# Kernel tuning notes

Measured on AMD Instinct MI355X. Metric: run time of the kernel, lower is better.

## Reference

```python
import jax, jax.numpy as jnp
import numpy as np

V = 100000   # num_regular_embeddings (full vocab)
K = 20000    # num custom (Poincare) embeddings
P = 300      # custom embedding dim
E = 256      # regular / output embedding dim
B = 1024
L = 256


def logmap0(v):
    # project from Poincare ball (c=1) to tangent space at origin
    norm = jnp.linalg.norm(v, axis=-1, keepdims=True)
    safe = jnp.where(norm > 0, norm, 0.5)            # avoid 0/0 and arctanh(0)/0
    scale = jnp.where(norm > 0, jnp.arctanh(safe) / safe, 1.0)
    return scale * v


def mobius_add(x, y):
    x2 = jnp.sum(x * x, axis=-1, keepdims=True)
    y2 = jnp.sum(y * y, axis=-1, keepdims=True)
    xy = jnp.sum(x * y, axis=-1, keepdims=True)
    num = (1 + 2 * xy + y2) * x + (1 - x2) * y
    denom = jnp.maximum(1 + 2 * xy + x2 * y2, 1e-15)
    return num / denom


def setup_inputs() -> dict:
    key = jax.random.key(0)
    k_x, k_perm, k_cw, k_rw, k_lw = jax.random.split(key, 5)

    x = jax.random.randint(k_x, (B, L), 0, V, dtype=jnp.int32)

    # K distinct custom vocab indices, excluding 0 (padding)
    custom_indices = jax.random.permutation(k_perm, jnp.arange(1, V, dtype=jnp.int32))[:K]

    # vocab -> custom table index (1..K), 0 for non-custom
    vocab_to_custom = jnp.zeros((V,), dtype=jnp.int32).at[custom_indices].set(
        jnp.arange(1, K + 1, dtype=jnp.int32))
    # vocab -> regular table index (0..V-K-1) for non-custom slots
    regular_vocab = jnp.where(vocab_to_custom == 0)[0]  # concrete, size V-K
    vocab_to_regular = jnp.zeros((V,), dtype=jnp.int32).at[regular_vocab].set(
        jnp.arange(V - K, dtype=jnp.int32))

    # fixed (pretrained, frozen) custom weights inside unit ball; row 0 = padding
    custom_fixed_w = (jax.random.normal(k_cw, (K + 1, P), dtype=jnp.float32) * 0.02).at[0].set(0.0)
    # trainable custom table initialized to zeros (as in the module)
    custom_train_w = jnp.zeros((K + 1, P), dtype=jnp.float32)
    # regular embedding table, row 0 = padding
    regular_w = (jax.random.normal(k_rw, (V - K, E), dtype=jnp.float32) * 0.02).at[0].set(0.0)
    # linear transform P -> E
    lin_w = jax.random.normal(k_lw, (E, P), dtype=jnp.float32) * 0.05
    lin_b = jnp.zeros((E,), dtype=jnp.float32)

    return {"x": x, "custom_indices": custom_indices,
            "vocab_to_custom": vocab_to_custom, "vocab_to_regular": vocab_to_regular,
            "custom_fixed_w": custom_fixed_w, "custom_train_w": custom_train_w,
            "regular_w": regular_w, "lin_w": lin_w, "lin_b": lin_b}


def reference(x, custom_indices, vocab_to_custom, vocab_to_regular,
              custom_fixed_w, custom_train_w, regular_w, lin_w, lin_b):
    mask = jnp.isin(x, custom_indices)                     # [B, L]
    custom_feat = jnp.where(mask, x, 0)
    regular_feat = jnp.where(mask, 0, x)

    cm = vocab_to_custom[custom_feat]                      # [B, L]
    fixed = logmap0(custom_fixed_w[cm])                    # [B, L, P]
    train = custom_train_w[cm]                             # [B, L, P]
    custom_emb = mobius_add(fixed, train)                  # [B, L, P]

    regular_emb = regular_w[vocab_to_regular[regular_feat]]  # [B, L, E]

    custom_emb = jnp.einsum("blp,ep->ble", custom_emb, lin_w) + lin_b
    return custom_emb + regular_emb
```

## Files before the change

kernel.cpp:

```cpp
#include <hip/hip_runtime.h>
#include <stdint.h>
#include <math.h>

#define NTOK (1024 * 256)
#define P_DIM 300
#define P_PAD 320
#define P_LDS 328
#define E_DIM 256

typedef __attribute__((ext_vector_type(8))) short bf16x8_t;
typedef __attribute__((ext_vector_type(4))) float f32x4_t;

__device__ __forceinline__ unsigned short f2b(float f) {
    union { float f; unsigned int i; } v; v.f = f;
    unsigned int x = v.i;
    return (unsigned short)((x + 0x7FFFu + ((x >> 16) & 1u)) >> 16);
}

__global__ __launch_bounds__(256) void k1_classify(
        const int* __restrict__ x, const int* __restrict__ v2c,
        const int* __restrict__ v2r,
        int* __restrict__ info, int* __restrict__ list, int* __restrict__ counter) {
    __shared__ int wb[4];
    int tid = threadIdx.x;
    int wid = tid >> 6;
    int lane = tid & 63;
    int base = blockIdx.x * 1024;

    int cmv[4], tv[4];
    unsigned long long bl[4];
    int wcnt = 0;
    #pragma unroll
    for (int it = 0; it < 4; it++) {
        int t = base + it * 256 + tid;
        int xv = x[t];
        int cm = v2c[xv];
        cmv[it] = cm; tv[it] = t;
        info[t] = (cm > 0) ? -cm : v2r[xv];
        bl[it] = __ballot(cm > 0);
        wcnt += __popcll(bl[it]);
    }
    if (lane == 0) wb[wid] = wcnt;
    __syncthreads();
    if (tid == 0) {
        int tot = wb[0] + wb[1] + wb[2] + wb[3];
        int b0 = atomicAdd(counter, tot);
        int p = b0;
        #pragma unroll
        for (int w = 0; w < 4; w++) { int c = wb[w]; wb[w] = p; p += c; }
    }
    __syncthreads();
    int off = wb[wid];
    unsigned long long lmask = (1ull << lane) - 1ull;
    #pragma unroll
    for (int it = 0; it < 4; it++) {
        if (cmv[it] > 0) {
            int pos = off + __popcll(bl[it] & lmask);
            list[pos] = tv[it];
        }
        off += __popcll(bl[it]);
    }
}

__global__ __launch_bounds__(256) void k2_base(
        const int* __restrict__ info,
        const float* __restrict__ regular_w,
        const float* __restrict__ lin_b,
        const float* __restrict__ lin_w,
        unsigned short* __restrict__ lin_w_pad,
        float* __restrict__ out) {
    int tid = threadIdx.x;
    if (blockIdx.x < (E_DIM * P_PAD) / 256) {
        int idx = blockIdx.x * 256 + tid;
        int e = idx / P_PAD;
        int k = idx - e * P_PAD;
        lin_w_pad[idx] = (k < P_DIM) ? f2b(lin_w[e * P_DIM + k]) : (unsigned short)0;
    }
    int lane = tid & 63;
    int wq = tid >> 6;
    float4 lb = *(const float4*)(lin_b + lane * 4);
    int base = blockIdx.x * 32;
    #pragma unroll
    for (int it = 0; it < 8; it++) {
        int t = base + wq * 8 + it;
        int inf = info[t];
        if (inf >= 0) {
            float4 rf = *(const float4*)(regular_w + (size_t)inf * E_DIM + lane * 4);
            float4 o;
            o.x = rf.x + lb.x; o.y = rf.y + lb.y;
            o.z = rf.z + lb.z; o.w = rf.w + lb.w;
            *(float4*)(out + (size_t)t * E_DIM + lane * 4) = o;
        }
    }
}

__global__ __launch_bounds__(256) void k3_gemm(
        const int* __restrict__ list, const int* __restrict__ counter,
        const int* __restrict__ info, const int* __restrict__ v2r,
        const float* __restrict__ fixed_w,
        const float* __restrict__ train_w,
        const unsigned short* __restrict__ lin_w_pad,
        const float* __restrict__ regular_w,
        const float* __restrict__ lin_b,
        float* __restrict__ out) {
    __shared__ __align__(16) unsigned short semb[32][P_LDS];
    int count = counter[0];
    int i0 = blockIdx.x * 32;
    if (i0 >= count) return;
    int tid = threadIdx.x;
    int wid = tid >> 6;
    int lane = tid & 63;

    for (int it = 0; it < 8; it++) {
        int i = i0 + wid * 8 + it;
        int iS = (i < count) ? i : (count - 1);
        int t = list[iS];
        int cm = -info[t];
        const float* fw = fixed_w + (size_t)cm * P_DIM;
        const float* tw = train_w + (size_t)cm * P_DIM;
        float w[5], tr[5];
        float sw2 = 0.f, st2 = 0.f, swt = 0.f;
        #pragma unroll
        for (int s = 0; s < 5; s++) {
            int j = lane + 64 * s;
            float wv = 0.f, tv = 0.f;
            if (j < P_DIM) { wv = fw[j]; tv = tw[j]; }
            w[s] = wv; tr[s] = tv;
            sw2 = fmaf(wv, wv, sw2); st2 = fmaf(tv, tv, st2); swt = fmaf(wv, tv, swt);
        }
        #pragma unroll
        for (int m = 32; m >= 1; m >>= 1) {
            sw2 += __shfl_xor(sw2, m, 64);
            st2 += __shfl_xor(st2, m, 64);
            swt += __shfl_xor(swt, m, 64);
        }
        float norm = sqrtf(sw2);
        norm = fminf(norm, 0.9999999f);
        float scale = (norm > 0.f) ? (atanhf(norm) / norm) : 1.0f;
        float x2 = scale * scale * sw2;
        float y2 = st2;
        float xy = scale * swt;
        float c1 = (1.f + 2.f * xy + y2) * scale;
        float c2 = (1.f - x2);
        float den = fmaxf(1.f + 2.f * xy + x2 * y2, 1e-15f);
        float inv = 1.f / den;
        int tl = wid * 8 + it;
        #pragma unroll
        for (int s = 0; s < 5; s++) {
            int j = lane + 64 * s;
            float v = (j < P_DIM) ? (c1 * w[s] + c2 * tr[s]) * inv : 0.f;
            semb[tl][j] = f2b(v);
        }
    }
    __syncthreads();

    int col = lane & 15;
    int kgrp = lane >> 4;
    int e0w = wid * 64;
    f32x4_t acc[2][4];
    #pragma unroll
    for (int a = 0; a < 2; a++)
        #pragma unroll
        for (int b = 0; b < 4; b++) acc[a][b] = (f32x4_t)(0.f);

    #pragma unroll
    for (int kk = 0; kk < 10; kk++) {
        int k0 = kk * 32 + kgrp * 8;
        bf16x8_t afr[2], bfr[4];
        #pragma unroll
        for (int mt = 0; mt < 2; mt++)
            afr[mt] = *(const bf16x8_t*)(&semb[mt * 16 + col][k0]);
        #pragma unroll
        for (int nt = 0; nt < 4; nt++) {
            int e = e0w + nt * 16 + col;
            bfr[nt] = *(const bf16x8_t*)(lin_w_pad + (size_t)e * P_PAD + k0);
        }
        #pragma unroll
        for (int mt = 0; mt < 2; mt++)
            #pragma unroll
            for (int nt = 0; nt < 4; nt++)
                acc[mt][nt] = __builtin_amdgcn_mfma_f32_16x16x32_bf16(
                    afr[mt], bfr[nt], acc[mt][nt], 0, 0, 0);
    }

    int rid0 = v2r[0];
    const float* rrow0 = regular_w + (size_t)rid0 * E_DIM;
    float lb[4];
    #pragma unroll
    for (int nt = 0; nt < 4; nt++) lb[nt] = lin_b[e0w + nt * 16 + col];
    int rbase = (lane >> 4) * 4;
    #pragma unroll
    for (int mt = 0; mt < 2; mt++) {
        #pragma unroll
        for (int r = 0; r < 4; r++) {
            int i = i0 + mt * 16 + rbase + r;
            if (i < count) {
                int t = list[i];
                float* orow = out + (size_t)t * E_DIM;
                #pragma unroll
                for (int nt = 0; nt < 4; nt++) {
                    int e = e0w + nt * 16 + col;
                    orow[e] = acc[mt][nt][r] + lb[nt] + rrow0[e];
                }
            }
        }
    }
}

extern "C" void kernel_launch(void* const* d_in, const int* in_sizes, int n_in,
                              void* d_out, int out_size, void* d_ws, size_t ws_size,
                              hipStream_t stream) {
    const int* x   = (const int*)d_in[0];
    const int* v2c = (const int*)d_in[2];
    const int* v2r = (const int*)d_in[3];
    const float* fixed_w   = (const float*)d_in[4];
    const float* train_w   = (const float*)d_in[5];
    const float* regular_w = (const float*)d_in[6];
    const float* lin_w     = (const float*)d_in[7];
    const float* lin_b     = (const float*)d_in[8];
    float* out = (float*)d_out;

    char* ws = (char*)d_ws;
    int* counter = (int*)ws;
    int* info    = (int*)(ws + 256);
    int* list    = (int*)(ws + 256 + 4 * (size_t)NTOK);
    unsigned short* lin_w_pad = (unsigned short*)(ws + 256 + 8 * (size_t)NTOK);

    hipMemsetAsync(counter, 0, 64, stream);
    k1_classify<<<NTOK / 1024, 256, 0, stream>>>(x, v2c, v2r, info, list, counter);
    k2_base<<<NTOK / 32, 256, 0, stream>>>(info, regular_w, lin_b, lin_w,
                                           lin_w_pad, out);
    k3_gemm<<<NTOK / 32, 256, 0, stream>>>(list, counter, info, v2r,
                                           fixed_w, train_w, lin_w_pad,
                                           regular_w, lin_b, out);
}
```

Before: 452.6 us.

## Fuse classify, regular gather and custom GEMM into one per-block kernel

New measurement: 542.7 us. +19.9%, slower.

```diff
diff --git a/kernel.cpp b/kernel.cpp
--- a/kernel.cpp
+++ b/kernel.cpp
@@ -3,6 +3,7 @@
 #include <math.h>
 
 #define NTOK (1024 * 256)
+#define TPB  128
 #define P_DIM 300
 #define P_PAD 320
 #define P_LDS 328
@@ -17,193 +18,167 @@
     return (unsigned short)((x + 0x7FFFu + ((x >> 16) & 1u)) >> 16);
 }
 
-__global__ __launch_bounds__(256) void k1_classify(
+__global__ __launch_bounds__(256) void k0_convert(
+        const float* __restrict__ lin_w, unsigned short* __restrict__ lin_w_pad) {
+    int idx = blockIdx.x * 256 + threadIdx.x;
+    int e = idx / P_PAD;
+    int k = idx - e * P_PAD;
+    lin_w_pad[idx] = (k < P_DIM) ? f2b(lin_w[(size_t)e * P_DIM + k]) : (unsigned short)0;
+}
+
+__global__ __launch_bounds__(256) void k_fused(
         const int* __restrict__ x, const int* __restrict__ v2c,
         const int* __restrict__ v2r,
-        int* __restrict__ info, int* __restrict__ list, int* __restrict__ counter) {
-    __shared__ int wb[4];
-    int tid = threadIdx.x;
-    int wid = tid >> 6;
-    int lane = tid & 63;
-    int base = blockIdx.x * 1024;
-
-    int cmv[4], tv[4];
-    unsigned long long bl[4];
-    int wcnt = 0;
-    #pragma unroll
-    for (int it = 0; it < 4; it++) {
-        int t = base + it * 256 + tid;
-        int xv = x[t];
-        int cm = v2c[xv];
-        cmv[it] = cm; tv[it] = t;
-        info[t] = (cm > 0) ? -cm : v2r[xv];
-        bl[it] = __ballot(cm > 0);
-        wcnt += __popcll(bl[it]);
-    }
-    if (lane == 0) wb[wid] = wcnt;
-    __syncthreads();
-    if (tid == 0) {
-        int tot = wb[0] + wb[1] + wb[2] + wb[3];
-        int b0 = atomicAdd(counter, tot);
-        int p = b0;
-        #pragma unroll
-        for (int w = 0; w < 4; w++) { int c = wb[w]; wb[w] = p; p += c; }
-    }
-    __syncthreads();
-    int off = wb[wid];
-    unsigned long long lmask = (1ull << lane) - 1ull;
-    #pragma unroll
-    for (int it = 0; it < 4; it++) {
-        if (cmv[it] > 0) {
-            int pos = off + __popcll(bl[it] & lmask);
-            list[pos] = tv[it];
-        }
-        off += __popcll(bl[it]);
-    }
-}
-
-__global__ __launch_bounds__(256) void k2_base(
-        const int* __restrict__ info,
-        const float* __restrict__ regular_w,
-        const float* __restrict__ lin_b,
-        const float* __restrict__ lin_w,
-        unsigned short* __restrict__ lin_w_pad,
-        float* __restrict__ out) {
-    int tid = threadIdx.x;
-    if (blockIdx.x < (E_DIM * P_PAD) / 256) {
-        int idx = blockIdx.x * 256 + tid;
-        int e = idx / P_PAD;
-        int k = idx - e * P_PAD;
-        lin_w_pad[idx] = (k < P_DIM) ? f2b(lin_w[e * P_DIM + k]) : (unsigned short)0;
-    }
-    int lane = tid & 63;
-    int wq = tid >> 6;
-    float4 lb = *(const float4*)(lin_b + lane * 4);
-    int base = blockIdx.x * 32;
-    #pragma unroll
-    for (int it = 0; it < 8; it++) {
-        int t = base + wq * 8 + it;
-        int inf = info[t];
-        if (inf >= 0) {
-            float4 rf = *(const float4*)(regular_w + (size_t)inf * E_DIM + lane * 4);
-            float4 o;
-            o.x = rf.x + lb.x; o.y = rf.y + lb.y;
-            o.z = rf.z + lb.z; o.w = rf.w + lb.w;
-            *(float4*)(out + (size_t)t * E_DIM + lane * 4) = o;
-        }
-    }
-}
-
-__global__ __launch_bounds__(256) void k3_gemm(
-        const int* __restrict__ list, const int* __restrict__ counter,
-        const int* __restrict__ info, const int* __restrict__ v2r,
         const float* __restrict__ fixed_w,
         const float* __restrict__ train_w,
+        const float* __restrict__ regular_w,
         const unsigned short* __restrict__ lin_w_pad,
-        const float* __restrict__ regular_w,
         const float* __restrict__ lin_b,
         float* __restrict__ out) {
     __shared__ __align__(16) unsigned short semb[32][P_LDS];
-    int count = counter[0];
-    int i0 = blockIdx.x * 32;
-    if (i0 >= count) return;
-    int tid = threadIdx.x;
-    int wid = tid >> 6;
+    __shared__ int stok[TPB];
+    __shared__ int scm[TPB];
+    __shared__ int rinfo[TPB];
+    __shared__ int s_n;
+
+    int tid  = threadIdx.x;
+    int wid  = tid >> 6;
     int lane = tid & 63;
-
-    for (int it = 0; it < 8; it++) {
-        int i = i0 + wid * 8 + it;
-        int iS = (i < count) ? i : (count - 1);
-        int t = list[iS];
-        int cm = -info[t];
-        const float* fw = fixed_w + (size_t)cm * P_DIM;
-        const float* tw = train_w + (size_t)cm * P_DIM;
-        float w[5], tr[5];
-        float sw2 = 0.f, st2 = 0.f, swt = 0.f;
-        #pragma unroll
-        for (int s = 0; s < 5; s++) {
-            int j = lane + 64 * s;
-            float wv = 0.f, tv = 0.f;
-            if (j < P_DIM) { wv = fw[j]; tv = tw[j]; }
-            w[s] = wv; tr[s] = tv;
-            sw2 = fmaf(wv, wv, sw2); st2 = fmaf(tv, tv, st2); swt = fmaf(wv, tv, swt);
-        }
-        #pragma unroll
-        for (int m = 32; m >= 1; m >>= 1) {
-            sw2 += __shfl_xor(sw2, m, 64);
-            st2 += __shfl_xor(st2, m, 64);
-            swt += __shfl_xor(swt, m, 64);
-        }
-        float norm = sqrtf(sw2);
-        norm = fminf(norm, 0.9999999f);
-        float scale = (norm > 0.f) ? (atanhf(norm) / norm) : 1.0f;
-        float x2 = scale * scale * sw2;
-        float y2 = st2;
-        float xy = scale * swt;
-        float c1 = (1.f + 2.f * xy + y2) * scale;
-        float c2 = (1.f - x2);
-        float den = fmaxf(1.f + 2.f * xy + x2 * y2, 1e-15f);
-        float inv = 1.f / den;
-        int tl = wid * 8 + it;
-        #pragma unroll
-        for (int s = 0; s < 5; s++) {
-            int j = lane + 64 * s;
-            float v = (j < P_DIM) ? (c1 * w[s] + c2 * tr[s]) * inv : 0.f;
-            semb[tl][j] = f2b(v);
-        }
-    }
+    int base = blockIdx.x * TPB;
+
+    if (tid == 0) s_n = 0;
     __syncthreads();
 
-    int col = lane & 15;
+    if (tid < TPB) {
+        int t  = base + tid;
+        int xv = x[t];
+        int cm = v2c[xv];
+        int ri = -1;
+        if (cm > 0) {
+            int p = atomicAdd(&s_n, 1);
+            stok[p] = t;
+            scm[p]  = cm;
+        } else {
+            ri = v2r[xv];
+        }
+        rinfo[tid] = ri;
+    }
+    __syncthreads();
+    int n = s_n;
+
+    f32x4_t lb4 = *(const f32x4_t*)(lin_b + lane * 4);
+    #pragma unroll 4
+    for (int it = 0; it < TPB / 4; it++) {
+        int li = wid * (TPB / 4) + it;
+        int ri = rinfo[li];
+        if (ri >= 0) {
+            f32x4_t rf = *(const f32x4_t*)(regular_w + (size_t)ri * E_DIM + lane * 4);
+            f32x4_t o = rf + lb4;
+            __builtin_nontemporal_store(
+                o, (f32x4_t*)(out + (size_t)(base + li) * E_DIM + lane * 4));
+        }
+    }
+
+    if (n == 0) return;
+
+    int col  = lane & 15;
     int kgrp = lane >> 4;
-    int e0w = wid * 64;
-    f32x4_t acc[2][4];
-    #pragma unroll
-    for (int a = 0; a < 2; a++)
-        #pragma unroll
-        for (int b = 0; b < 4; b++) acc[a][b] = (f32x4_t)(0.f);
-
-    #pragma unroll
-    for (int kk = 0; kk < 10; kk++) {
-        int k0 = kk * 32 + kgrp * 8;
-        bf16x8_t afr[2], bfr[4];
-        #pragma unroll
-        for (int mt = 0; mt < 2; mt++)
-            afr[mt] = *(const bf16x8_t*)(&semb[mt * 16 + col][k0]);
-        #pragma unroll
-        for (int nt = 0; nt < 4; nt++) {
-            int e = e0w + nt * 16 + col;
-            bfr[nt] = *(const bf16x8_t*)(lin_w_pad + (size_t)e * P_PAD + k0);
-        }
-        #pragma unroll
-        for (int mt = 0; mt < 2; mt++)
-            #pragma unroll
-            for (int nt = 0; nt < 4; nt++)
-                acc[mt][nt] = __builtin_amdgcn_mfma_f32_16x16x32_bf16(
-                    afr[mt], bfr[nt], acc[mt][nt], 0, 0, 0);
-    }
-
+    int e0w  = wid * 64;
+    int rbase = kgrp * 4;
+    float lbe[4], rr0[4];
     int rid0 = v2r[0];
     const float* rrow0 = regular_w + (size_t)rid0 * E_DIM;
-    float lb[4];
     #pragma unroll
-    for (int nt = 0; nt < 4; nt++) lb[nt] = lin_b[e0w + nt * 16 + col];
-    int rbase = (lane >> 4) * 4;
-    #pragma unroll
-    for (int mt = 0; mt < 2; mt++) {
+    for (int nt = 0; nt < 4; nt++) {
+        lbe[nt] = lin_b[e0w + nt * 16 + col];
+        rr0[nt] = rrow0[e0w + nt * 16 + col];
+    }
+
+    for (int c0 = 0; c0 < n; c0 += 32) {
+        int cn = n - c0; if (cn > 32) cn = 32;
+
+        for (int i = wid; i < cn; i += 4) {
+            int cm = scm[c0 + i];
+            const float* fw = fixed_w + (size_t)cm * P_DIM;
+            const float* tw = train_w + (size_t)cm * P_DIM;
+            float w[5], tr[5];
+            float sw2 = 0.f, st2 = 0.f, swt = 0.f;
+            #pragma unroll
+            for (int s = 0; s < 5; s++) {
+                int j = lane + 64 * s;
+                float wv = 0.f, tv = 0.f;
+                if (j < P_DIM) { wv = fw[j]; tv = tw[j]; }
+                w[s] = wv; tr[s] = tv;
+                sw2 = fmaf(wv, wv, sw2); st2 = fmaf(tv, tv, st2); swt = fmaf(wv, tv, swt);
+            }
+            #pragma unroll
+            for (int m = 32; m >= 1; m >>= 1) {
+                sw2 += __shfl_xor(sw2, m, 64);
+                st2 += __shfl_xor(st2, m, 64);
+                swt += __shfl_xor(swt, m, 64);
+            }
+            float norm = sqrtf(sw2);
+            norm = fminf(norm, 0.9999999f);
+            float scale = (norm > 0.f) ? (atanhf(norm) / norm) : 1.0f;
+            float x2 = scale * scale * sw2;
+            float y2 = st2;
+            float xy = scale * swt;
+            float c1 = (1.f + 2.f * xy + y2) * scale;
+            float c2 = (1.f - x2);
+            float den = fmaxf(1.f + 2.f * xy + x2 * y2, 1e-15f);
+            float inv = 1.f / den;
+            #pragma unroll
+            for (int s = 0; s < 5; s++) {
+                int j = lane + 64 * s;
+                float v = (j < P_DIM) ? (c1 * w[s] + c2 * tr[s]) * inv : 0.f;
+                semb[i][j] = f2b(v);
+            }
+        }
+        __syncthreads();
+
+        f32x4_t acc[2][4];
         #pragma unroll
-        for (int r = 0; r < 4; r++) {
-            int i = i0 + mt * 16 + rbase + r;
-            if (i < count) {
-                int t = list[i];
-                float* orow = out + (size_t)t * E_DIM;
+        for (int a = 0; a < 2; a++)
+            #pragma unroll
+            for (int b = 0; b < 4; b++) acc[a][b] = (f32x4_t)(0.f);
+
+        #pragma unroll
+        for (int kk = 0; kk < 10; kk++) {
+            int k0 = kk * 32 + kgrp * 8;
+            bf16x8_t afr[2], bfr[4];
+            afr[0] = *(const bf16x8_t*)(&semb[col][k0]);
+            afr[1] = *(const bf16x8_t*)(&semb[16 + col][k0]);
+            #pragma unroll
+            for (int nt = 0; nt < 4; nt++) {
+                int e = e0w + nt * 16 + col;
+                bfr[nt] = *(const bf16x8_t*)(lin_w_pad + (size_t)e * P_PAD + k0);
+            }
+            #pragma unroll
+            for (int mt = 0; mt < 2; mt++)
                 #pragma unroll
-                for (int nt = 0; nt < 4; nt++) {
-                    int e = e0w + nt * 16 + col;
-                    orow[e] = acc[mt][nt][r] + lb[nt] + rrow0[e];
+                for (int nt = 0; nt < 4; nt++)
+                    acc[mt][nt] = __builtin_amdgcn_mfma_f32_16x16x32_bf16(
+                        afr[mt], bfr[nt], acc[mt][nt], 0, 0, 0);
+        }
+
+        #pragma unroll
+        for (int mt = 0; mt < 2; mt++) {
+            #pragma unroll
+            for (int r = 0; r < 4; r++) {
+                int row = mt * 16 + rbase + r;
+                if (row < cn) {
+                    int t = stok[c0 + row];
+                    float* orow = out + (size_t)t * E_DIM;
+                    #pragma unroll
+                    for (int nt = 0; nt < 4; nt++) {
+                        __builtin_nontemporal_store(
+                            acc[mt][nt][r] + lbe[nt] + rr0[nt],
+                            orow + e0w + nt * 16 + col);
+                    }
                 }
             }
         }
+        __syncthreads();
     }
 }
 
@@ -220,17 +195,9 @@
     const float* lin_b     = (const float*)d_in[8];
     float* out = (float*)d_out;
 
-    char* ws = (char*)d_ws;
-    int* counter = (int*)ws;
-    int* info    = (int*)(ws + 256);
-    int* list    = (int*)(ws + 256 + 4 * (size_t)NTOK);
-    unsigned short* lin_w_pad = (unsigned short*)(ws + 256 + 8 * (size_t)NTOK);
-
-    hipMemsetAsync(counter, 0, 64, stream);
-    k1_classify<<<NTOK / 1024, 256, 0, stream>>>(x, v2c, v2r, info, list, counter);
-    k2_base<<<NTOK / 32, 256, 0, stream>>>(info, regular_w, lin_b, lin_w,
-                                           lin_w_pad, out);
-    k3_gemm<<<NTOK / 32, 256, 0, stream>>>(list, counter, info, v2r,
-                                           fixed_w, train_w, lin_w_pad,
-                                           regular_w, lin_b, out);
-}
+    unsigned short* lin_w_pad = (unsigned short*)d_ws;
+
+    k0_convert<<<(E_DIM * P_PAD) / 256, 256, 0, stream>>>(lin_w, lin_w_pad);
+    k_fused<<<NTOK / TPB, 256, 0, stream>>>(x, v2c, v2r, fixed_w, train_w,
+                                            regular_w, lin_w_pad, lin_b, out);
+}
```
